# Performance work log

Hardware: AMD Instinct MI355X
Metric: run time of the kernel (lower is better)

Reference implementation:

```python
import jax, jax.numpy as jnp
import numpy as np

N = 16384
K = 4096  # codebook_size
D = 512   # embedding_dim
COMMITMENT_COST = 0.25


def setup_inputs() -> dict:
    key = jax.random.key(0)
    kz, kc = jax.random.split(key)
    z = jax.random.normal(kz, (N, D), dtype=jnp.float32)
    # nn.Embedding weight init: uniform(-1/K, 1/K)
    codebook = jax.random.uniform(kc, (K, D), dtype=jnp.float32,
                                  minval=-1.0 / K, maxval=1.0 / K)
    return {"z": z, "codebook": codebook}


def reference(z, codebook):
    # squared L2 distances: [N, K]
    dists = (jnp.sum(z * z, axis=1, keepdims=True)
             + jnp.sum(codebook * codebook, axis=1)
             - 2.0 * jnp.matmul(z, codebook.T))
    idx = jnp.argmin(dists, axis=1)                 # [N]
    z_q = codebook[idx]                             # gather == one-hot @ codebook
    # straight-through estimator
    z_q_ste = z + jax.lax.stop_gradient(z_q - z)
    commitment_loss = jnp.mean((jax.lax.stop_gradient(z) - z_q) ** 2)
    codebook_loss = jnp.mean((z - jax.lax.stop_gradient(z_q)) ** 2)
    loss = codebook_loss + COMMITMENT_COST * commitment_loss
    encoding_indices = idx[:, None]                 # [N, 1] to match torch shape
    return (z_q_ste, encoding_indices, loss)
```

## Files before the change

### kernel.cpp

```cpp
#include <hip/hip_runtime.h>
#include <math.h>

#define N_ROWS 16384
#define K_CODES 4096
#define D_DIM 512
#define NCHUNK 8
#define KCHUNK (K_CODES / NCHUNK)
#define MARGIN 2.5e-3f
#define CCAP 32

typedef unsigned int uint32;
typedef unsigned short u16t;
typedef __attribute__((ext_vector_type(8))) short short8;
typedef __attribute__((ext_vector_type(4))) float f32x4;

__device__ __forceinline__ float fmul_(float a, float b) { return __fmul_rn(a, b); }
__device__ __forceinline__ float fadd_(float a, float b) { return __fadd_rn(a, b); }

__global__ void rownorm_np_kernel(const float* __restrict__ src, int nrows,
                                  float* __restrict__ out) {
    int gid = blockIdx.x * blockDim.x + threadIdx.x;
    int row = gid >> 2;
    int blk = gid & 3;
    if (row >= nrows) return;
    const float4* p = (const float4*)(src + (size_t)row * D_DIM + blk * 128);
    float4 v0 = p[0], v1 = p[1];
    float r0 = fmul_(v0.x, v0.x), r1 = fmul_(v0.y, v0.y);
    float r2 = fmul_(v0.z, v0.z), r3 = fmul_(v0.w, v0.w);
    float r4 = fmul_(v1.x, v1.x), r5 = fmul_(v1.y, v1.y);
    float r6 = fmul_(v1.z, v1.z), r7 = fmul_(v1.w, v1.w);
#pragma unroll
    for (int i = 1; i < 16; i++) {
        float4 w0 = p[2 * i], w1 = p[2 * i + 1];
        r0 = fadd_(r0, fmul_(w0.x, w0.x));
        r1 = fadd_(r1, fmul_(w0.y, w0.y));
        r2 = fadd_(r2, fmul_(w0.z, w0.z));
        r3 = fadd_(r3, fmul_(w0.w, w0.w));
        r4 = fadd_(r4, fmul_(w1.x, w1.x));
        r5 = fadd_(r5, fmul_(w1.y, w1.y));
        r6 = fadd_(r6, fmul_(w1.z, w1.z));
        r7 = fadd_(r7, fmul_(w1.w, w1.w));
    }
    float s = fadd_(fadd_(fadd_(r0, r1), fadd_(r2, r3)),
                    fadd_(fadd_(r4, r5), fadd_(r6, r7)));
    float u = __shfl_down(s, 1, 64);
    float t = fadd_(s, u);
    float w = __shfl_down(t, 2, 64);
    float tot = fadd_(t, w);
    if (blk == 0) out[row] = tot;
}

__device__ __forceinline__ u16t f2bf(float x) {
    uint32 u = __float_as_uint(x);
    return (u16t)((u + 0x7fffu + ((u >> 16) & 1u)) >> 16);
}
__device__ __forceinline__ uint32 fkey(float f) {
    uint32 u = __float_as_uint(f);
    return (u & 0x80000000u) ? ~u : (u | 0x80000000u);
}
__device__ __forceinline__ float fdec(uint32 k) {
    uint32 u = (k & 0x80000000u) ? (k ^ 0x80000000u) : ~k;
    return __uint_as_float(u);
}
__device__ __forceinline__ float dpp_min16(float x) {
    int y;
    y = __builtin_amdgcn_update_dpp(0, __float_as_int(x), 0xB1, 0xf, 0xf, true);
    x = fminf(x, __int_as_float(y));
    y = __builtin_amdgcn_update_dpp(0, __float_as_int(x), 0x4E, 0xf, 0xf, true);
    x = fminf(x, __int_as_float(y));
    y = __builtin_amdgcn_update_dpp(0, __float_as_int(x), 0x141, 0xf, 0xf, true);
    x = fminf(x, __int_as_float(y));
    y = __builtin_amdgcn_update_dpp(0, __float_as_int(x), 0x140, 0xf, 0xf, true);
    x = fminf(x, __int_as_float(y));
    return x;
}

__global__ void cvt_bf16_kernel(const float* __restrict__ src,
                                u16t* __restrict__ dst, int n4) {
    int i = blockIdx.x * blockDim.x + threadIdx.x;
    if (i >= n4) return;
    float4 v = ((const float4*)src)[i];
    ushort4 o;
    o.x = f2bf(v.x); o.y = f2bf(v.y); o.z = f2bf(v.z); o.w = f2bf(v.w);
    ((ushort4*)dst)[i] = o;
}

__global__ __launch_bounds__(512, 4) void score_gemm_kernel(
    const u16t* __restrict__ zb, const u16t* __restrict__ cbb,
    const float* __restrict__ cnorm,
    float* __restrict__ chunkmin,
    uint32* __restrict__ cnts,
    uint2* __restrict__ cand) {
    __shared__ alignas(16) u16t Ab[128 * 32];
    __shared__ alignas(16) u16t Bb[128 * 32];
    __shared__ uint32 rowminU[128];
    __shared__ int ccnt[128];

    const int t = threadIdx.x;
    const int bx = blockIdx.x;
    const int by = blockIdx.y;
    const int row0 = by * 128, k0 = bx * KCHUNK;
    const int w = t >> 6, lane = t & 63;
    const int wx = w & 1, wy = w >> 1;
    const int l15 = lane & 15, quad = lane >> 4;

    if (t < 128) { rowminU[t] = 0xFFFFFFFFu; ccnt[t] = 0; }

    for (int kt = 0; kt < 4; kt++) {
        f32x4 acc[2][4];
#pragma unroll
        for (int i = 0; i < 2; i++)
#pragma unroll
            for (int j = 0; j < 4; j++) acc[i][j] = (f32x4){0.f, 0.f, 0.f, 0.f};

        const u16t* ga = zb + (size_t)(row0 + (t >> 2)) * D_DIM + (t & 3) * 8;
        const u16t* gb = cbb + (size_t)(k0 + kt * 128 + (t >> 2)) * D_DIM + (t & 3) * 8;

        for (int dt = 0; dt < 16; dt++) {
            __syncthreads();
            __builtin_amdgcn_global_load_lds(
                (const __attribute__((address_space(1))) void*)ga,
                (__attribute__((address_space(3))) void*)((char*)Ab + w * 1024),
                16, 0, 0);
            __builtin_amdgcn_global_load_lds(
                (const __attribute__((address_space(1))) void*)gb,
                (__attribute__((address_space(3))) void*)((char*)Bb + w * 1024),
                16, 0, 0);
            ga += 32; gb += 32;
            __syncthreads();
            short8 a[2];
#pragma unroll
            for (int i = 0; i < 2; i++)
                a[i] = *(const short8*)((char*)Ab + (wy * 32 + i * 16 + l15) * 64 + quad * 16);
#pragma unroll
            for (int j = 0; j < 4; j++) {
                short8 b = *(const short8*)((char*)Bb + (wx * 64 + j * 16 + l15) * 64 + quad * 16);
#pragma unroll
                for (int i = 0; i < 2; i++)
                    acc[i][j] = __builtin_amdgcn_mfma_f32_16x16x32_bf16(a[i], b, acc[i][j], 0, 0, 0);
            }
        }

        float cnj[4];
#pragma unroll
        for (int j = 0; j < 4; j++)
            cnj[j] = cnorm[k0 + kt * 128 + wx * 64 + j * 16 + l15];

#pragma unroll
        for (int i = 0; i < 2; i++) {
#pragma unroll
            for (int r = 0; r < 4; r++) {
                float m = fmaf(-2.f, acc[i][0][r], cnj[0]);
                m = fminf(m, fmaf(-2.f, acc[i][1][r], cnj[1]));
                m = fminf(m, fmaf(-2.f, acc[i][2][r], cnj[2]));
                m = fminf(m, fmaf(-2.f, acc[i][3][r], cnj[3]));
                m = dpp_min16(m);
                if (l15 == 0)
                    atomicMin(&rowminU[wy * 32 + i * 16 + quad * 4 + r], fkey(m));
            }
        }
        __syncthreads();
#pragma unroll
        for (int i = 0; i < 2; i++) {
#pragma unroll
            for (int r = 0; r < 4; r++) {
                const int rl = wy * 32 + i * 16 + quad * 4 + r;
                const float thr = fdec(rowminU[rl]) + MARGIN;
#pragma unroll
                for (int j = 0; j < 4; j++) {
                    float s = fmaf(-2.f, acc[i][j][r], cnj[j]);
                    if (s <= thr) {
                        int pos = atomicAdd(&ccnt[rl], 1);
                        if (pos < CCAP) {
                            uint2 e;
                            e.x = __float_as_uint(s);
                            e.y = (uint32)(k0 + kt * 128 + wx * 64 + j * 16 + l15);
                            cand[((size_t)(row0 + rl) * NCHUNK + bx) * CCAP + pos] = e;
                        }
                    }
                }
            }
        }
    }
    __syncthreads();
    if (t < 128) {
        chunkmin[(size_t)(row0 + t) * NCHUNK + bx] = fdec(rowminU[t]);
        int c = ccnt[t];
        cnts[(size_t)(row0 + t) * NCHUNK + bx] = (uint32)(c < CCAP ? c : CCAP);
    }
}

__global__ __launch_bounds__(256) void refine_kernel(
    const uint2* __restrict__ cand, const uint32* __restrict__ cnts,
    const float* __restrict__ chunkmin,
    const float* __restrict__ z, const float* __restrict__ cb,
    const float* __restrict__ zz, const float* __restrict__ cnorm,
    float* __restrict__ out_zq, float* __restrict__ out_idx,
    float* __restrict__ rowsum) {
    const int t = threadIdx.x;
    const int wid = t >> 6, lane = t & 63;
    const int row = blockIdx.x * 4 + wid;

    float cm = chunkmin[(size_t)row * NCHUNK + (lane & 7)];
    cm = fminf(cm, __shfl_xor(cm, 1, 64));
    cm = fminf(cm, __shfl_xor(cm, 2, 64));
    cm = fminf(cm, __shfl_xor(cm, 4, 64));
    const float thr = cm + MARGIN;

    const float* zr = z + (size_t)row * D_DIM;
    float4 z0 = *(const float4*)(zr + lane * 8);
    float4 z1 = *(const float4*)(zr + lane * 8 + 4);
    const float zzr = zz[row];

    float bv = 3.4e38f;
    int bi = 0x7fffffff;
#pragma unroll
    for (int it = 0; it < (NCHUNK * CCAP) / 64; ++it) {
        int idx = it * 64 + lane;
        int c = idx >> 5, s2 = idx & (CCAP - 1);
        uint32 n = cnts[(size_t)row * NCHUNK + c];
        int kk = -1;
        if ((uint32)s2 < n) {
            uint2 e = cand[((size_t)row * NCHUNK + c) * CCAP + s2];
            if (__uint_as_float(e.x) <= thr) kk = (int)e.y;
        }
        unsigned long long mask = __ballot(kk >= 0);
        while (mask) {
            int src = __ffsll((unsigned long long)mask) - 1;
            mask &= (mask - 1);
            int k = __shfl(kk, src, 64);
            const float* cr = cb + (size_t)k * D_DIM;
            float4 c0 = *(const float4*)(cr + lane * 8);
            float4 c1 = *(const float4*)(cr + lane * 8 + 4);
            float d = fmul_(z0.x, c0.x);
            d = fmaf(z0.y, c0.y, d); d = fmaf(z0.z, c0.z, d); d = fmaf(z0.w, c0.w, d);
            d = fmaf(z1.x, c1.x, d); d = fmaf(z1.y, c1.y, d);
            d = fmaf(z1.z, c1.z, d); d = fmaf(z1.w, c1.w, d);
#pragma unroll
            for (int off = 1; off < 64; off <<= 1)
                d = fadd_(d, __shfl_xor(d, off, 64));
            float dist = fmaf(-2.f, d, fadd_(zzr, cnorm[k]));
            if (dist < bv || (dist == bv && k < bi)) { bv = dist; bi = k; }
        }
    }
    if (bi == 0x7fffffff) bi = 0;
    if (lane == 0) out_idx[row] = (float)bi;

    const float* cq = cb + (size_t)bi * D_DIM;
    float v[4];
#pragma unroll
    for (int q = 0; q < 4; q++) {
        const int off = q * 128 + lane * 2;
        float2 zv2 = *(const float2*)(zr + off);
        float2 cv2 = *(const float2*)(cq + off);
        float2 o;
        o.x = fadd_(zv2.x, __fsub_rn(cv2.x, zv2.x));
        o.y = fadd_(zv2.y, __fsub_rn(cv2.y, zv2.y));
        *(float2*)(out_zq + (size_t)row * D_DIM + off) = o;
        float dx = zv2.x - cv2.x, dy = zv2.y - cv2.y;
        v[q] = dx * dx + dy * dy;
    }
    float s = fadd_(fadd_(v[0], v[2]), fadd_(v[1], v[3]));
    s = fadd_(s, __shfl_down(s, 32, 64));
    s = fadd_(s, __shfl_down(s, 16, 64));
    s = fadd_(s, __shfl_down(s, 8, 64));
    s = fadd_(s, __shfl_down(s, 4, 64));
    s = fadd_(s, __shfl_down(s, 2, 64));
    s = fadd_(s, __shfl_down(s, 1, 64));
    if (lane == 0) rowsum[row] = s;
}

__global__ void loss_kernel(const float* __restrict__ rowsum,
                            float* __restrict__ out_loss) {
    __shared__ float sm[256];
    float s = 0.f;
    for (int i = threadIdx.x; i < N_ROWS; i += 256) s += rowsum[i];
    sm[threadIdx.x] = s;
    __syncthreads();
    for (int st = 128; st; st >>= 1) {
        if (threadIdx.x < st) sm[threadIdx.x] += sm[threadIdx.x + st];
        __syncthreads();
    }
    if (threadIdx.x == 0)
        *out_loss = 1.25f * sm[0] / (float)(N_ROWS * D_DIM);
}

#define BM 128
#define BN 128
#define BK 16
#define TM 8
#define TN 8

__global__ __launch_bounds__(256, 4) void vq_argmin_kernel(
    const float* __restrict__ z, const float* __restrict__ cb,
    const float* __restrict__ zz, const float* __restrict__ cnorm,
    float* __restrict__ pval, int* __restrict__ pidx) {
    __shared__ float As[BK][BM + 4];
    __shared__ float Bs[BK][BN + 4];
    __shared__ float rv[BM][17];
    __shared__ int   ri[BM][17];

    const int bx = blockIdx.x;
    const int by = blockIdx.y;
    const int row0 = by * BM;
    const int k0 = bx * KCHUNK;
    const int t = threadIdx.x;
    const int tx = t & 15;
    const int ty = t >> 4;

    float minv[TM];
    int   mini[TM];
#pragma unroll
    for (int i = 0; i < TM; i++) { minv[i] = 3.4e38f; mini[i] = 0; }
    float zrow[TM];
#pragma unroll
    for (int i = 0; i < TM; i++) zrow[i] = zz[row0 + ty * TM + i];
    const int sr = t >> 1;
    const int sdq = (t & 1) * 8;

    for (int kt = 0; kt < KCHUNK / BN; kt++) {
        const int col0 = k0 + kt * BN;
        float acc[TM][TN];
#pragma unroll
        for (int i = 0; i < TM; i++)
#pragma unroll
            for (int j = 0; j < TN; j++) acc[i][j] = 0.f;
        for (int dt = 0; dt < D_DIM; dt += BK) {
            {
                const float* src = z + (size_t)(row0 + sr) * D_DIM + dt + sdq;
                float4 v0 = *(const float4*)(src);
                float4 v1 = *(const float4*)(src + 4);
                As[sdq + 0][sr] = v0.x; As[sdq + 1][sr] = v0.y;
                As[sdq + 2][sr] = v0.z; As[sdq + 3][sr] = v0.w;
                As[sdq + 4][sr] = v1.x; As[sdq + 5][sr] = v1.y;
                As[sdq + 6][sr] = v1.z; As[sdq + 7][sr] = v1.w;
                const float* srcb = cb + (size_t)(col0 + sr) * D_DIM + dt + sdq;
                float4 w0 = *(const float4*)(srcb);
                float4 w1 = *(const float4*)(srcb + 4);
                Bs[sdq + 0][sr] = w0.x; Bs[sdq + 1][sr] = w0.y;
                Bs[sdq + 2][sr] = w0.z; Bs[sdq + 3][sr] = w0.w;
                Bs[sdq + 4][sr] = w1.x; Bs[sdq + 5][sr] = w1.y;
                Bs[sdq + 6][sr] = w1.z; Bs[sdq + 7][sr] = w1.w;
            }
            __syncthreads();
#pragma unroll
            for (int d = 0; d < BK; d++) {
                float a[TM], b[TN];
#pragma unroll
                for (int i = 0; i < TM; i++) a[i] = As[d][ty * TM + i];
#pragma unroll
                for (int j = 0; j < TN; j++) b[j] = Bs[d][tx * TN + j];
#pragma unroll
                for (int i = 0; i < TM; i++)
#pragma unroll
                    for (int j = 0; j < TN; j++)
                        acc[i][j] = fmaf(a[i], b[j], acc[i][j]);
            }
            __syncthreads();
        }
#pragma unroll
        for (int j = 0; j < TN; j++) {
            const int col = col0 + tx * TN + j;
            const float cn = cnorm[col];
#pragma unroll
            for (int i = 0; i < TM; i++) {
                float s1 = fadd_(zrow[i], cn);
                float s = fmaf(-2.f, acc[i][j], s1);
                if (s < minv[i]) { minv[i] = s; mini[i] = col; }
            }
        }
    }
#pragma unroll
    for (int i = 0; i < TM; i++) {
        rv[ty * TM + i][tx] = minv[i];
        ri[ty * TM + i][tx] = mini[i];
    }
    __syncthreads();
    if (t < BM) {
        float bv = rv[t][0];
        int   bi = ri[t][0];
#pragma unroll
        for (int x = 1; x < 16; x++) {
            float v = rv[t][x]; int ii = ri[t][x];
            if (v < bv || (v == bv && ii < bi)) { bv = v; bi = ii; }
        }
        pval[(size_t)(row0 + t) * NCHUNK + bx] = bv;
        pidx[(size_t)(row0 + t) * NCHUNK + bx] = bi;
    }
}

__global__ void finalize_kernel(const float* __restrict__ z,
                                const float* __restrict__ cb,
                                const float* __restrict__ pval,
                                const int* __restrict__ pidx,
                                float* __restrict__ out_zq,
                                float* __restrict__ out_idx,
                                float* __restrict__ rowsum) {
    int row = (blockIdx.x * blockDim.x + threadIdx.x) >> 6;
    int lane = threadIdx.x & 63;
    if (row >= N_ROWS) return;
    float bv = pval[(size_t)row * NCHUNK];
    int   bi = pidx[(size_t)row * NCHUNK];
#pragma unroll
    for (int c = 1; c < NCHUNK; c++) {
        float v = pval[(size_t)row * NCHUNK + c];
        int  ii = pidx[(size_t)row * NCHUNK + c];
        if (v < bv || (v == bv && ii < bi)) { bv = v; bi = ii; }
    }
    const float4* zr = (const float4*)(z + (size_t)row * D_DIM);
    const float4* cr = (const float4*)(cb + (size_t)bi * D_DIM);
    float4* orow = (float4*)(out_zq + (size_t)row * D_DIM);
    float s = 0.f;
#pragma unroll
    for (int i = 0; i < 2; i++) {
        float4 zv = zr[i * 64 + lane];
        float4 cv = cr[i * 64 + lane];
        float4 o;
        o.x = fadd_(zv.x, __fsub_rn(cv.x, zv.x));
        o.y = fadd_(zv.y, __fsub_rn(cv.y, zv.y));
        o.z = fadd_(zv.z, __fsub_rn(cv.z, zv.z));
        o.w = fadd_(zv.w, __fsub_rn(cv.w, zv.w));
        orow[i * 64 + lane] = o;
        float dx = zv.x - cv.x, dy = zv.y - cv.y;
        float dz = zv.z - cv.z, dw = zv.w - cv.w;
        s += dx * dx + dy * dy + dz * dz + dw * dw;
    }
#pragma unroll
    for (int off = 32; off; off >>= 1) s += __shfl_down(s, off, 64);
    if (lane == 0) {
        rowsum[row] = s;
        out_idx[row] = (float)bi;
    }
}

extern "C" void kernel_launch(void* const* d_in, const int* in_sizes, int n_in,
                              void* d_out, int out_size, void* d_ws, size_t ws_size,
                              hipStream_t stream) {
    const float* z  = (const float*)d_in[0];
    const float* cb = (const float*)d_in[1];
    float* out      = (float*)d_out;
    float* out_zq   = out;
    float* out_idx  = out + (size_t)N_ROWS * D_DIM;
    float* out_loss = out_idx + N_ROWS;

    float* zz     = (float*)d_ws;
    float* cnorm  = zz + N_ROWS;
    float* rowsum = cnorm + K_CODES;
    u16t*  z_bf   = (u16t*)(rowsum + N_ROWS);
    u16t*  cb_bf  = z_bf + (size_t)N_ROWS * D_DIM;
    float* chunkmin = (float*)(cb_bf + (size_t)K_CODES * D_DIM);
    uint32* cnts  = (uint32*)(chunkmin + (size_t)N_ROWS * NCHUNK);
    uint2* cand   = (uint2*)(cnts + (size_t)N_ROWS * NCHUNK);
    const size_t WS_NEEDED = (size_t)(N_ROWS + K_CODES + N_ROWS) * 4
                           + (size_t)N_ROWS * D_DIM * 2
                           + (size_t)K_CODES * D_DIM * 2
                           + (size_t)N_ROWS * NCHUNK * 4 * 2
                           + (size_t)N_ROWS * NCHUNK * CCAP * 8;

    if (ws_size >= WS_NEEDED) {
        cvt_bf16_kernel<<<(N_ROWS * D_DIM / 4 + 255) / 256, 256, 0, stream>>>(z, z_bf, N_ROWS * D_DIM / 4);
        cvt_bf16_kernel<<<(K_CODES * D_DIM / 4 + 255) / 256, 256, 0, stream>>>(cb, cb_bf, K_CODES * D_DIM / 4);
        rownorm_np_kernel<<<(N_ROWS * 4) / 256, 256, 0, stream>>>(z, N_ROWS, zz);
        rownorm_np_kernel<<<(K_CODES * 4) / 256, 256, 0, stream>>>(cb, K_CODES, cnorm);

        dim3 g1(NCHUNK, N_ROWS / 128);
        score_gemm_kernel<<<g1, 512, 0, stream>>>(z_bf, cb_bf, cnorm,
                                                  chunkmin, cnts, cand);
        refine_kernel<<<N_ROWS / 4, 256, 0, stream>>>(cand, cnts, chunkmin,
                                                      z, cb, zz, cnorm,
                                                      out_zq, out_idx, rowsum);
        loss_kernel<<<1, 256, 0, stream>>>(rowsum, out_loss);
    } else {
        float* pval = rowsum + N_ROWS;
        int*   pidx = (int*)(pval + (size_t)N_ROWS * NCHUNK);
        rownorm_np_kernel<<<(N_ROWS * 4) / 256, 256, 0, stream>>>(z, N_ROWS, zz);
        rownorm_np_kernel<<<(K_CODES * 4) / 256, 256, 0, stream>>>(cb, K_CODES, cnorm);
        dim3 g2(NCHUNK, N_ROWS / BM);
        vq_argmin_kernel<<<g2, 256, 0, stream>>>(z, cb, zz, cnorm, pval, pidx);
        finalize_kernel<<<N_ROWS / 4, 256, 0, stream>>>(z, cb, pval, pidx,
                                                        out_zq, out_idx, rowsum);
        loss_kernel<<<1, 256, 0, stream>>>(rowsum, out_loss);
    }
}
```

Measured before the change: 286.5 us.

## Fuse bf16 conversion with row norms and double the GEMM K-step per barrier

Replaces the two bf16 conversion kernels and two row-norm kernels with one prep kernel that reads each row once, writes its bf16 copy and computes its squared norm. This removes three launches and a second full read of z and the codebook. The score GEMM now stages 64 elements of D per sync step instead of 32, which halves the number of barrier pairs and doubles the LDS tile size. The larger LDS footprint may limit how many blocks fit per CU.

```diff
diff --git a/kernel.cpp b/kernel.cpp
--- a/kernel.cpp
+++ b/kernel.cpp
@@ -16,6 +16,96 @@
 
 __device__ __forceinline__ float fmul_(float a, float b) { return __fmul_rn(a, b); }
 __device__ __forceinline__ float fadd_(float a, float b) { return __fadd_rn(a, b); }
+
+__device__ __forceinline__ u16t f2bf(float x) {
+    uint32 u = __float_as_uint(x);
+    return (u16t)((u + 0x7fffu + ((u >> 16) & 1u)) >> 16);
+}
+__device__ __forceinline__ uint32 fkey(float f) {
+    uint32 u = __float_as_uint(f);
+    return (u & 0x80000000u) ? ~u : (u | 0x80000000u);
+}
+__device__ __forceinline__ float fdec(uint32 k) {
+    uint32 u = (k & 0x80000000u) ? (k ^ 0x80000000u) : ~k;
+    return __uint_as_float(u);
+}
+__device__ __forceinline__ float dpp_min16(float x) {
+    int y;
+    y = __builtin_amdgcn_update_dpp(0, __float_as_int(x), 0xB1, 0xf, 0xf, true);
+    x = fminf(x, __int_as_float(y));
+    y = __builtin_amdgcn_update_dpp(0, __float_as_int(x), 0x4E, 0xf, 0xf, true);
+    x = fminf(x, __int_as_float(y));
+    y = __builtin_amdgcn_update_dpp(0, __float_as_int(x), 0x141, 0xf, 0xf, true);
+    x = fminf(x, __int_as_float(y));
+    y = __builtin_amdgcn_update_dpp(0, __float_as_int(x), 0x140, 0xf, 0xf, true);
+    x = fminf(x, __int_as_float(y));
+    return x;
+}
+
+__global__ void prep_kernel(const float* __restrict__ z,
+                            const float* __restrict__ cb,
+                            u16t* __restrict__ z_bf, u16t* __restrict__ cb_bf,
+                            float* __restrict__ zz, float* __restrict__ cnorm) {
+    int gid = blockIdx.x * blockDim.x + threadIdx.x;
+    int row = gid >> 2;
+    int blk = gid & 3;
+    const float* src;
+    u16t* dst;
+    float* outn;
+    if (row < N_ROWS) {
+        src = z + (size_t)row * D_DIM;
+        dst = z_bf + (size_t)row * D_DIM;
+        outn = zz + row;
+    } else {
+        int r = row - N_ROWS;
+        if (r >= K_CODES) return;
+        src = cb + (size_t)r * D_DIM;
+        dst = cb_bf + (size_t)r * D_DIM;
+        outn = cnorm + r;
+    }
+    const float4* p = (const float4*)(src + blk * 128);
+    u16t* d = dst + blk * 128;
+    float4 v0 = p[0], v1 = p[1];
+    {
+        short8 o;
+        o[0] = (short)f2bf(v0.x); o[1] = (short)f2bf(v0.y);
+        o[2] = (short)f2bf(v0.z); o[3] = (short)f2bf(v0.w);
+        o[4] = (short)f2bf(v1.x); o[5] = (short)f2bf(v1.y);
+        o[6] = (short)f2bf(v1.z); o[7] = (short)f2bf(v1.w);
+        *(short8*)d = o;
+    }
+    float r0 = fmul_(v0.x, v0.x), r1 = fmul_(v0.y, v0.y);
+    float r2 = fmul_(v0.z, v0.z), r3 = fmul_(v0.w, v0.w);
+    float r4 = fmul_(v1.x, v1.x), r5 = fmul_(v1.y, v1.y);
+    float r6 = fmul_(v1.z, v1.z), r7 = fmul_(v1.w, v1.w);
+#pragma unroll
+    for (int i = 1; i < 16; i++) {
+        float4 w0 = p[2 * i], w1 = p[2 * i + 1];
+        {
+            short8 o;
+            o[0] = (short)f2bf(w0.x); o[1] = (short)f2bf(w0.y);
+            o[2] = (short)f2bf(w0.z); o[3] = (short)f2bf(w0.w);
+            o[4] = (short)f2bf(w1.x); o[5] = (short)f2bf(w1.y);
+            o[6] = (short)f2bf(w1.z); o[7] = (short)f2bf(w1.w);
+            *(short8*)(d + i * 8) = o;
+        }
+        r0 = fadd_(r0, fmul_(w0.x, w0.x));
+        r1 = fadd_(r1, fmul_(w0.y, w0.y));
+        r2 = fadd_(r2, fmul_(w0.z, w0.z));
+        r3 = fadd_(r3, fmul_(w0.w, w0.w));
+        r4 = fadd_(r4, fmul_(w1.x, w1.x));
+        r5 = fadd_(r5, fmul_(w1.y, w1.y));
+        r6 = fadd_(r6, fmul_(w1.z, w1.z));
+        r7 = fadd_(r7, fmul_(w1.w, w1.w));
+    }
+    float s = fadd_(fadd_(fadd_(r0, r1), fadd_(r2, r3)),
+                    fadd_(fadd_(r4, r5), fadd_(r6, r7)));
+    float u = __shfl_down(s, 1, 64);
+    float t = fadd_(s, u);
+    float w = __shfl_down(t, 2, 64);
+    float tot = fadd_(t, w);
+    if (blk == 0) *outn = tot;
+}
 
 __global__ void rownorm_np_kernel(const float* __restrict__ src, int nrows,
                                   float* __restrict__ out) {
@@ -50,49 +140,14 @@
     if (blk == 0) out[row] = tot;
 }
 
-__device__ __forceinline__ u16t f2bf(float x) {
-    uint32 u = __float_as_uint(x);
-    return (u16t)((u + 0x7fffu + ((u >> 16) & 1u)) >> 16);
-}
-__device__ __forceinline__ uint32 fkey(float f) {
-    uint32 u = __float_as_uint(f);
-    return (u & 0x80000000u) ? ~u : (u | 0x80000000u);
-}
-__device__ __forceinline__ float fdec(uint32 k) {
-    uint32 u = (k & 0x80000000u) ? (k ^ 0x80000000u) : ~k;
-    return __uint_as_float(u);
-}
-__device__ __forceinline__ float dpp_min16(float x) {
-    int y;
-    y = __builtin_amdgcn_update_dpp(0, __float_as_int(x), 0xB1, 0xf, 0xf, true);
-    x = fminf(x, __int_as_float(y));
-    y = __builtin_amdgcn_update_dpp(0, __float_as_int(x), 0x4E, 0xf, 0xf, true);
-    x = fminf(x, __int_as_float(y));
-    y = __builtin_amdgcn_update_dpp(0, __float_as_int(x), 0x141, 0xf, 0xf, true);
-    x = fminf(x, __int_as_float(y));
-    y = __builtin_amdgcn_update_dpp(0, __float_as_int(x), 0x140, 0xf, 0xf, true);
-    x = fminf(x, __int_as_float(y));
-    return x;
-}
-
-__global__ void cvt_bf16_kernel(const float* __restrict__ src,
-                                u16t* __restrict__ dst, int n4) {
-    int i = blockIdx.x * blockDim.x + threadIdx.x;
-    if (i >= n4) return;
-    float4 v = ((const float4*)src)[i];
-    ushort4 o;
-    o.x = f2bf(v.x); o.y = f2bf(v.y); o.z = f2bf(v.z); o.w = f2bf(v.w);
-    ((ushort4*)dst)[i] = o;
-}
-
 __global__ __launch_bounds__(512, 4) void score_gemm_kernel(
     const u16t* __restrict__ zb, const u16t* __restrict__ cbb,
     const float* __restrict__ cnorm,
     float* __restrict__ chunkmin,
     uint32* __restrict__ cnts,
     uint2* __restrict__ cand) {
-    __shared__ alignas(16) u16t Ab[128 * 32];
-    __shared__ alignas(16) u16t Bb[128 * 32];
+    __shared__ alignas(16) u16t Ab[128 * 64];
+    __shared__ alignas(16) u16t Bb[128 * 64];
     __shared__ uint32 rowminU[128];
     __shared__ int ccnt[128];
 
@@ -116,28 +171,41 @@
         const u16t* ga = zb + (size_t)(row0 + (t >> 2)) * D_DIM + (t & 3) * 8;
         const u16t* gb = cbb + (size_t)(k0 + kt * 128 + (t >> 2)) * D_DIM + (t & 3) * 8;
 
-        for (int dt = 0; dt < 16; dt++) {
+        for (int dt = 0; dt < 8; dt++) {
             __syncthreads();
             __builtin_amdgcn_global_load_lds(
                 (const __attribute__((address_space(1))) void*)ga,
                 (__attribute__((address_space(3))) void*)((char*)Ab + w * 1024),
                 16, 0, 0);
             __builtin_amdgcn_global_load_lds(
+                (const __attribute__((address_space(1))) void*)(ga + 32),
+                (__attribute__((address_space(3))) void*)((char*)Ab + 8192 + w * 1024),
+                16, 0, 0);
+            __builtin_amdgcn_global_load_lds(
                 (const __attribute__((address_space(1))) void*)gb,
                 (__attribute__((address_space(3))) void*)((char*)Bb + w * 1024),
                 16, 0, 0);
-            ga += 32; gb += 32;
+            __builtin_amdgcn_global_load_lds(
+                (const __attribute__((address_space(1))) void*)(gb + 32),
+                (__attribute__((address_space(3))) void*)((char*)Bb + 8192 + w * 1024),
+                16, 0, 0);
+            ga += 64; gb += 64;
             __syncthreads();
-            short8 a[2];
-#pragma unroll
-            for (int i = 0; i < 2; i++)
-                a[i] = *(const short8*)((char*)Ab + (wy * 32 + i * 16 + l15) * 64 + quad * 16);
-#pragma unroll
-            for (int j = 0; j < 4; j++) {
-                short8 b = *(const short8*)((char*)Bb + (wx * 64 + j * 16 + l15) * 64 + quad * 16);
+#pragma unroll
+            for (int sub = 0; sub < 2; sub++) {
+                short8 a[2];
 #pragma unroll
                 for (int i = 0; i < 2; i++)
-                    acc[i][j] = __builtin_amdgcn_mfma_f32_16x16x32_bf16(a[i], b, acc[i][j], 0, 0, 0);
+                    a[i] = *(const short8*)((char*)Ab + sub * 8192 +
+                                            (wy * 32 + i * 16 + l15) * 64 + quad * 16);
+#pragma unroll
+                for (int j = 0; j < 4; j++) {
+                    short8 b = *(const short8*)((char*)Bb + sub * 8192 +
+                                                (wx * 64 + j * 16 + l15) * 64 + quad * 16);
+#pragma unroll
+                    for (int i = 0; i < 2; i++)
+                        acc[i][j] = __builtin_amdgcn_mfma_f32_16x16x32_bf16(a[i], b, acc[i][j], 0, 0, 0);
+                }
             }
         }
 
@@ -458,10 +526,8 @@
                            + (size_t)N_ROWS * NCHUNK * CCAP * 8;
 
     if (ws_size >= WS_NEEDED) {
-        cvt_bf16_kernel<<<(N_ROWS * D_DIM / 4 + 255) / 256, 256, 0, stream>>>(z, z_bf, N_ROWS * D_DIM / 4);
-        cvt_bf16_kernel<<<(K_CODES * D_DIM / 4 + 255) / 256, 256, 0, stream>>>(cb, cb_bf, K_CODES * D_DIM / 4);
-        rownorm_np_kernel<<<(N_ROWS * 4) / 256, 256, 0, stream>>>(z, N_ROWS, zz);
-        rownorm_np_kernel<<<(K_CODES * 4) / 256, 256, 0, stream>>>(cb, K_CODES, cnorm);
+        prep_kernel<<<((N_ROWS + K_CODES) * 4) / 256, 256, 0, stream>>>(
+            z, cb, z_bf, cb_bf, zz, cnorm);
 
         dim3 g1(NCHUNK, N_ROWS / 128);
         score_gemm_kernel<<<g1, 512, 0, stream>>>(z_bf, cb_bf, cnorm,
```

Result: faster. 276.2 us (-3.6%).
